# Optimization experiments

Hardware: AMD Instinct MI355X
Metric: run time of the kernel (lower is better)

The kernel has to match this reference:

```python
import jax, jax.numpy as jnp
import numpy as np

EPS = 1e-6        # vn_layers EPS
BN_EPS = 1e-5     # torch BatchNorm eps
NEG = 0.2         # leaky relu negative_slope


def _bcast(v, nd):
    return v.reshape((1, -1) + (1,) * (nd - 2))


def vn_linear_leaky(x, W, D, gamma, beta):
    """VNLinearLeakyReLU: x [B,Cin,3,...], W/D [Cout,Cin] -> [B,Cout,3,...]."""
    p = jnp.einsum('oc,bcv...->bov...', W, x)
    # VNBatchNorm (training-mode batch statistics) on vector norms
    norm = jnp.linalg.norm(p, axis=2) + EPS              # [B,Cout,...]
    axes = (0,) + tuple(range(2, norm.ndim))
    mu = jnp.mean(norm, axis=axes, keepdims=True)
    var = jnp.mean((norm - mu) ** 2, axis=axes, keepdims=True)
    norm_bn = (norm - mu) / jnp.sqrt(var + BN_EPS)
    norm_bn = norm_bn * _bcast(gamma, norm.ndim) + _bcast(beta, norm.ndim)
    p = p / norm[:, :, None] * norm_bn[:, :, None]
    # VN LeakyReLU against learned direction d
    d = jnp.einsum('oc,bcv...->bov...', D, x)
    dot = jnp.sum(p * d, axis=2, keepdims=True)
    mask = (dot >= 0).astype(p.dtype)
    dns = jnp.sum(d * d, axis=2, keepdims=True)
    return NEG * p + (1 - NEG) * (mask * p + (1 - mask) * (p - (dot / (dns + EPS)) * d))


def chnorm(x):
    """channel_equi_vec_normalize: x [B,C,3,...]."""
    n = jnp.linalg.norm(x, axis=2, keepdims=True)        # [B,C,1,...]
    x_dir = x / jnp.maximum(n, 1e-12)
    n_ch = jnp.linalg.norm(n, axis=1, keepdims=True)     # normalize norms over channels
    return x_dir * (n / jnp.maximum(n_ch, 1e-12))


def get_graph_feature(y, k):
    """VN-DGCNN graph feature: y [B,C,3,N] -> [B,2C,3,N,K]."""
    B, C, _, N = y.shape
    yp = jnp.transpose(y, (0, 3, 1, 2))                  # [B,N,C,3]
    flat = yp.reshape(B, N, 3 * C)
    sq = jnp.sum(flat * flat, axis=-1)                   # [B,N]
    inner = jnp.einsum('bnd,bmd->bnm', flat, flat)
    neg_dist = 2 * inner - sq[:, :, None] - sq[:, None, :]
    _, idx = jax.lax.top_k(neg_dist, k)                  # [B,N,K] nearest (incl. self)
    nbr = jax.vmap(lambda pts, ids: pts[ids])(yp, idx)   # [B,N,K,C,3]
    ctr = jnp.broadcast_to(yp[:, :, None], (B, N, k, C, 3))
    feat = jnp.concatenate([nbr - ctr, ctr], axis=3)     # [B,N,K,2C,3]
    return jnp.transpose(feat, (0, 3, 4, 1, 2))


def reference(x, y, Wq, Dq, gq, bq, Wk, Dk, gk, bk, Wv, Dv, gv, bv, k):
    Qx = chnorm(vn_linear_leaky(x, Wq, Dq, gq, bq))      # [B,C,3,N]
    yg = get_graph_feature(y, k)                         # [B,2C,3,N,K]
    Ky = chnorm(vn_linear_leaky(yg, Wk, Dk, gk, bk))     # [B,C,3,N,K]
    Vy = vn_linear_leaky(yg, Wv, Dv, gv, bv)             # [B,C,3,N,K]
    qk = jnp.sum(Ky * Qx[..., None], axis=2)             # [B,C,N,K]
    C = qk.shape[1]
    atten = jax.nn.softmax(qk / jnp.sqrt(jnp.float32(3 * C)), axis=-1)
    return x + jnp.sum(atten[:, :, None] * Vy, axis=-1)  # [B,C,3,N]


def setup_inputs() -> dict:
    key = jax.random.key(0)
    B, C, N, K = 4, 64, 2048, 16
    ks = jax.random.split(key, 8)
    s1 = 1.0 / np.sqrt(C)
    s2 = 1.0 / np.sqrt(2 * C)
    return {
        'x': jax.random.normal(ks[0], (B, C, 3, N), jnp.float32),
        'y': jax.random.normal(ks[1], (B, C, 3, N), jnp.float32),
        'Wq': jax.random.normal(ks[2], (C, C), jnp.float32) * s1,
        'Dq': jax.random.normal(ks[3], (C, C), jnp.float32) * s1,
        'gq': jnp.ones((C,), jnp.float32),
        'bq': jnp.zeros((C,), jnp.float32),
        'Wk': jax.random.normal(ks[4], (C, 2 * C), jnp.float32) * s2,
        'Dk': jax.random.normal(ks[5], (C, 2 * C), jnp.float32) * s2,
        'gk': jnp.ones((C,), jnp.float32),
        'bk': jnp.zeros((C,), jnp.float32),
        'Wv': jax.random.normal(ks[6], (C, 2 * C), jnp.float32) * s2,
        'Dv': jax.random.normal(ks[7], (C, 2 * C), jnp.float32) * s2,
        'gv': jnp.ones((C,), jnp.float32),
        'bv': jnp.zeros((C,), jnp.float32),
        'k': K,
    }
```

## Files before the change

### kernel.cpp

```cpp
#include <hip/hip_runtime.h>
#include <cstdint>
#include <cstddef>

constexpr int B_ = 4, C_ = 64, N_ = 2048, K_ = 16;
constexpr int D3 = 192;
constexpr float EPS_ = 1e-6f, BNE_ = 1e-5f, NEG_ = 0.2f;
constexpr size_t S_ = (size_t)B_ * N_ * D3;

constexpr size_t OFF_PQ  = 0;
constexpr size_t OFF_DQ  = 1*S_;
constexpr size_t OFF_UK  = 2*S_;
constexpr size_t OFF_WK  = 3*S_;
constexpr size_t OFF_UDK = 4*S_;
constexpr size_t OFF_WDK = 5*S_;
constexpr size_t OFF_UV  = 6*S_;
constexpr size_t OFF_WV  = 7*S_;
constexpr size_t OFF_UDV = 8*S_;
constexpr size_t OFF_WDV = 9*S_;
constexpr size_t OFF_SQ  = 10*S_;
constexpr size_t OFF_ST  = OFF_SQ + (size_t)B_*N_;
constexpr size_t OFF_IDX = OFF_ST + 1024;
constexpr size_t OFF_DIST= OFF_IDX + (size_t)B_*N_*K_;

__device__ __forceinline__ float wred_sum(float v) {
  #pragma unroll
  for (int off = 32; off > 0; off >>= 1) v += __shfl_xor(v, off, 64);
  return v;
}

__device__ __forceinline__ void vnlk(float& p0, float& p1, float& p2,
                                     float d0, float d1, float d2,
                                     float s, float sh) {
  float n2 = p0*p0 + p1*p1 + p2*p2;
  float norm = __builtin_amdgcn_sqrtf(n2) + EPS_;
  float f = fmaf(norm, s, sh) * __builtin_amdgcn_rcpf(norm);
  p0 *= f; p1 *= f; p2 *= f;
  float dot = p0*d0 + p1*d1 + p2*d2;
  float dns = d0*d0 + d1*d1 + d2*d2;
  float g = (1.f - NEG_) * fminf(dot, 0.f) * __builtin_amdgcn_rcpf(dns + EPS_);
  p0 = fmaf(-g, d0, p0); p1 = fmaf(-g, d1, p1); p2 = fmaf(-g, d2, p2);
}

__device__ __forceinline__ float chnorm_sc(float nc, float nch) {
  return nc * __builtin_amdgcn_rcpf(fmaxf(nc, 1e-12f))
            * __builtin_amdgcn_rcpf(fmaxf(nch, 1e-12f));
}

template<bool PAIR>
__device__ __forceinline__ void do_mm(const float (*ys)[36], const float (*Wl)[129],
                                      float* __restrict__ out0, float* __restrict__ out1,
                                      float* s1s, float* s2s, bool qs,
                                      int og, int ng, int b, int n0) {
  float accU[4][2][3] = {};
  float accW[4][2][3] = {};
  #pragma unroll 4
  for (int c = 0; c < 64; ++c) {
    float w1[4], wd[4];
    #pragma unroll
    for (int i = 0; i < 4; ++i) {
      w1[i] = Wl[og*4 + i][c];
      if (PAIR) wd[i] = Wl[og*4 + i][64 + c] - w1[i];
    }
    #pragma unroll
    for (int jj = 0; jj < 2; ++jj)
      #pragma unroll
      for (int v = 0; v < 3; ++v) {
        float yv = ys[c*3 + v][ng*2 + jj];
        #pragma unroll
        for (int i = 0; i < 4; ++i) {
          accU[i][jj][v] = fmaf(w1[i], yv, accU[i][jj][v]);
          if (PAIR) accW[i][jj][v] = fmaf(wd[i], yv, accW[i][jj][v]);
        }
      }
  }
  #pragma unroll
  for (int jj = 0; jj < 2; ++jj) {
    int n = n0 + ng*2 + jj;
    size_t base = ((size_t)b*N_ + n)*D3 + og*12;
    alignas(16) float tmp[12];
    #pragma unroll
    for (int i = 0; i < 4; ++i)
      #pragma unroll
      for (int v = 0; v < 3; ++v) tmp[i*3+v] = accU[i][jj][v];
    float4* dst = (float4*)(out0 + base);
    dst[0] = ((float4*)tmp)[0]; dst[1] = ((float4*)tmp)[1]; dst[2] = ((float4*)tmp)[2];
    if (PAIR) {
      #pragma unroll
      for (int i = 0; i < 4; ++i)
        #pragma unroll
        for (int v = 0; v < 3; ++v) tmp[i*3+v] = accW[i][jj][v];
      float4* dst1 = (float4*)(out1 + base);
      dst1[0] = ((float4*)tmp)[0]; dst1[1] = ((float4*)tmp)[1]; dst1[2] = ((float4*)tmp)[2];
    }
  }
  if (!PAIR && qs) {
    #pragma unroll
    for (int i = 0; i < 4; ++i) {
      float a = 0.f, b2 = 0.f;
      #pragma unroll
      for (int jj = 0; jj < 2; ++jj) {
        float nn = sqrtf(accU[i][jj][0]*accU[i][jj][0] + accU[i][jj][1]*accU[i][jj][1]
                       + accU[i][jj][2]*accU[i][jj][2]) + EPS_;
        a += nn; b2 += nn*nn;
      }
      atomicAdd(&s1s[og*4 + i], a);
      atomicAdd(&s2s[og*4 + i], b2);
    }
  }
}

__global__ __launch_bounds__(256) void transform_kernel(
    const float* __restrict__ x, const float* __restrict__ y,
    const float* __restrict__ Wq, const float* __restrict__ Dq,
    const float* __restrict__ Wk, const float* __restrict__ Dk,
    const float* __restrict__ Wv, const float* __restrict__ Dv,
    float* __restrict__ ws) {
  __shared__ float ys[D3][36];
  __shared__ float Wl[64][129];
  __shared__ float s1s[64], s2s[64];
  int t = threadIdx.x, n0 = blockIdx.x*32, b = blockIdx.y, z = blockIdx.z;
  const bool isx = (z < 2);
  const float* in = (isx ? x : y) + (size_t)b*D3*N_;
  #pragma unroll
  for (int i = 0; i < 6; ++i) {
    int lin = t + i*256;
    int d = lin >> 3, c4 = (lin & 7)*4;
    *(float4*)&ys[d][c4] = *(const float4*)&in[(size_t)d*N_ + n0 + c4];
  }
  const float* Wg = (z==0)?Wq:(z==1)?Dq:(z==2)?Wk:(z==3)?Dk:(z==4)?Wv:Dv;
  if (isx) { for (int i = t; i < 4096; i += 256) Wl[i>>6][i&63] = Wg[i]; }
  else     { for (int i = t; i < 8192; i += 256) Wl[i>>7][i&127] = Wg[i]; }
  if (z == 0 && t < 64) { s1s[t] = 0.f; s2s[t] = 0.f; }
  __syncthreads();
  if (z == 2 && t < 32) {
    float s = 0.f;
    for (int d = 0; d < D3; ++d) { float v = ys[d][t]; s += v*v; }
    ws[OFF_SQ + (size_t)b*N_ + n0 + t] = s;
  }
  int og = t & 15, ng = t >> 4;
  float* st = ws + OFF_ST;
  if (isx) {
    float* out0 = ws + (z ? OFF_DQ : OFF_PQ);
    do_mm<false>(ys, Wl, out0, nullptr, s1s, s2s, z == 0, og, ng, b, n0);
    if (z == 0) {
      __syncthreads();
      if (t < 64) { atomicAdd(&st[t], s1s[t]); atomicAdd(&st[64 + t], s2s[t]); }
    }
  } else {
    float* out0 = ws + ((z==2)?OFF_UK:(z==3)?OFF_UDK:(z==4)?OFF_UV:OFF_UDV);
    float* out1 = ws + ((z==2)?OFF_WK:(z==3)?OFF_WDK:(z==4)?OFF_WV:OFF_WDV);
    do_mm<true>(ys, Wl, out0, out1, nullptr, nullptr, false, og, ng, b, n0);
  }
}

__global__ __launch_bounds__(256) void dist_kernel(const float* __restrict__ y,
                                                   float* __restrict__ ws,
                                                   int b0, size_t dstride) {
  __shared__ float As[32][68];
  __shared__ float Bs[32][136];
  int b = b0 + blockIdx.z;
  const float* yb = y + (size_t)b * D3 * N_;
  const float* sq = ws + OFF_SQ + (size_t)b * N_;
  float* dist = ws + OFF_DIST + dstride * blockIdx.z;
  int t = threadIdx.x;
  int m0 = blockIdx.x * 128, n0 = blockIdx.y * 64;
  int tm = t & 15, tn = t >> 4;
  float acc[4][8] = {};
  for (int dt = 0; dt < 6; ++dt) {
    __syncthreads();
    #pragma unroll
    for (int i = 0; i < 2; ++i) {
      int idx = t + i*256;
      int dd = idx >> 4, c4 = (idx & 15)*4;
      *(float4*)&As[dd][c4] = *(const float4*)&yb[(size_t)(dt*32 + dd)*N_ + n0 + c4];
    }
    #pragma unroll
    for (int i = 0; i < 4; ++i) {
      int idx = t + i*256;
      int dd = idx >> 5, c4 = (idx & 31)*4;
      *(float4*)&Bs[dd][c4] = *(const float4*)&yb[(size_t)(dt*32 + dd)*N_ + m0 + c4];
    }
    __syncthreads();
    #pragma unroll 8
    for (int dd = 0; dd < 32; ++dd) {
      float4 a4 = *(float4*)&As[dd][tn*4];
      float4 b4 = *(float4*)&Bs[dd][tm*4];
      float4 c4 = *(float4*)&Bs[dd][64 + tm*4];
      float ar[4] = {a4.x, a4.y, a4.z, a4.w};
      float b0v[4] = {b4.x, b4.y, b4.z, b4.w};
      float b1v[4] = {c4.x, c4.y, c4.z, c4.w};
      #pragma unroll
      for (int j = 0; j < 4; ++j) {
        #pragma unroll
        for (int i = 0; i < 4; ++i) {
          acc[j][i]   = fmaf(ar[j], b0v[i], acc[j][i]);
          acc[j][4+i] = fmaf(ar[j], b1v[i], acc[j][4+i]);
        }
      }
    }
  }
  float4 s0 = *(const float4*)&sq[m0 + tm*4];
  float4 s1 = *(const float4*)&sq[m0 + 64 + tm*4];
  float sm0[4] = {s0.x, s0.y, s0.z, s0.w};
  float sm1[4] = {s1.x, s1.y, s1.z, s1.w};
  #pragma unroll
  for (int j = 0; j < 4; ++j) {
    float sn = sq[n0 + tn*4 + j];
    float4 r0, r1;
    r0.x = 2.f*acc[j][0] - sn - sm0[0]; r0.y = 2.f*acc[j][1] - sn - sm0[1];
    r0.z = 2.f*acc[j][2] - sn - sm0[2]; r0.w = 2.f*acc[j][3] - sn - sm0[3];
    r1.x = 2.f*acc[j][4] - sn - sm1[0]; r1.y = 2.f*acc[j][5] - sn - sm1[1];
    r1.z = 2.f*acc[j][6] - sn - sm1[2]; r1.w = 2.f*acc[j][7] - sn - sm1[3];
    size_t rowb = (size_t)(n0 + tn*4 + j)*N_ + m0 + tm*4;
    *(float4*)&dist[rowb]      = r0;
    *(float4*)&dist[rowb + 64] = r1;
  }
}

__global__ __launch_bounds__(256) void topk_kernel(const float* __restrict__ ws_c,
                                                   int* __restrict__ idxo,
                                                   int b0, size_t dstride) {
  int t = threadIdx.x;
  int w = t >> 6, l = t & 63;
  int n = blockIdx.x*4 + w;
  int b = b0 + blockIdx.y;
  const float* dr = ws_c + OFF_DIST + dstride*blockIdx.y + (size_t)n * N_;
  float v[32];
  #pragma unroll
  for (int j = 0; j < 32; ++j) v[j] = dr[j*64 + l];
  int mine = 0;
  for (int it = 0; it < K_; ++it) {
    float bv = v[0]; int bj = 0;
    #pragma unroll
    for (int j = 1; j < 32; ++j) {
      bool g = v[j] > bv;
      bv = g ? v[j] : bv;
      bj = g ? j : bj;
    }
    int bm = bj*64 + l;
    #pragma unroll
    for (int off = 32; off > 0; off >>= 1) {
      float ov = __shfl_xor(bv, off, 64);
      int   om = __shfl_xor(bm, off, 64);
      if (ov > bv || (ov == bv && om < bm)) { bv = ov; bm = om; }
    }
    if (l == it) mine = bm;
    int wj = bm >> 6, wl = bm & 63;
    #pragma unroll
    for (int j = 0; j < 32; ++j)
      v[j] = (j == wj && l == wl) ? -3.4e38f : v[j];
  }
  if (l < K_) idxo[((size_t)b*N_ + n)*K_ + l] = mine;
}

__global__ __launch_bounds__(256) void kvstats_kernel(float* __restrict__ ws,
                                                      const int* __restrict__ idxp) {
  int t = threadIdx.x, o = t & 63, eg = t >> 6;
  int e0 = blockIdx.x * 128, b = blockIdx.y;
  const float* uK = ws + OFF_UK; const float* wK = ws + OFF_WK;
  const float* uV = ws + OFF_UV; const float* wV = ws + OFF_WV;
  int bN = b * N_;
  float k1 = 0.f, k2 = 0.f, v1 = 0.f, v2 = 0.f;
  for (int j = 0; j < 32; ++j) {
    int e = e0 + eg + j*4;
    int n = e >> 4, kk = e & 15;
    int m = idxp[(bN + n)*K_ + kk];
    int rb = (bN + n)*D3 + o*3;
    int gb = (bN + m)*D3 + o*3;
    float p0 = uK[gb] + wK[rb], p1 = uK[gb+1] + wK[rb+1], p2 = uK[gb+2] + wK[rb+2];
    float nk = __builtin_amdgcn_sqrtf(p0*p0 + p1*p1 + p2*p2) + EPS_;
    k1 += nk; k2 += nk*nk;
    float q0 = uV[gb] + wV[rb], q1 = uV[gb+1] + wV[rb+1], q2 = uV[gb+2] + wV[rb+2];
    float nv = __builtin_amdgcn_sqrtf(q0*q0 + q1*q1 + q2*q2) + EPS_;
    v1 += nv; v2 += nv*nv;
  }
  __shared__ float red[4][256];
  red[0][t] = k1; red[1][t] = k2; red[2][t] = v1; red[3][t] = v2;
  __syncthreads();
  if (t < 64) {
    float* st = ws + OFF_ST;
    float a = red[0][t] + red[0][t+64] + red[0][t+128] + red[0][t+192];
    atomicAdd(&st[128 + t], a);
    a = red[1][t] + red[1][t+64] + red[1][t+128] + red[1][t+192];
    atomicAdd(&st[192 + t], a);
    a = red[2][t] + red[2][t+64] + red[2][t+128] + red[2][t+192];
    atomicAdd(&st[256 + t], a);
    a = red[3][t] + red[3][t+64] + red[3][t+128] + red[3][t+192];
    atomicAdd(&st[320 + t], a);
  }
}

__global__ void bn_finalize(const float* __restrict__ gq, const float* __restrict__ bq,
                            const float* __restrict__ gk, const float* __restrict__ bk,
                            const float* __restrict__ gv, const float* __restrict__ bv,
                            float* __restrict__ ws) {
  int o = threadIdx.x;
  if (o >= 64) return;
  float* st = ws + OFF_ST;
  float cq = (float)(B_ * N_);
  float mu = st[o] / cq;
  float var = fmaxf(st[64+o]/cq - mu*mu, 0.f);
  float s = gq[o] * rsqrtf(var + BNE_);
  st[384+o] = s; st[448+o] = bq[o] - mu*s;
  float ck = (float)(B_ * N_ * K_);
  mu = st[128+o] / ck;
  var = fmaxf(st[192+o]/ck - mu*mu, 0.f);
  s = gk[o] * rsqrtf(var + BNE_);
  st[512+o] = s; st[576+o] = bk[o] - mu*s;
  mu = st[256+o] / ck;
  var = fmaxf(st[320+o]/ck - mu*mu, 0.f);
  s = gv[o] * rsqrtf(var + BNE_);
  st[640+o] = s; st[704+o] = bv[o] - mu*s;
}

__global__ __launch_bounds__(256, 2) void final_kernel(const float* __restrict__ x,
                                                       const float* __restrict__ ws_c,
                                                       const int* __restrict__ idxp,
                                                       float* __restrict__ out) {
  const float* pq  = ws_c + OFF_PQ;  const float* dq  = ws_c + OFF_DQ;
  const float* uK  = ws_c + OFF_UK;  const float* wK  = ws_c + OFF_WK;
  const float* uDk = ws_c + OFF_UDK; const float* wDk = ws_c + OFF_WDK;
  const float* uV  = ws_c + OFF_UV;  const float* wV  = ws_c + OFF_WV;
  const float* uDv = ws_c + OFF_UDV; const float* wDv = ws_c + OFF_WDV;
  const float* st  = ws_c + OFF_ST;
  int t = threadIdx.x, o = t & 63, w = t >> 6;
  int n0 = blockIdx.x*4, n = n0 + w, b = blockIdx.y;
  int bN = b * N_;
  __shared__ float ob2[192][5];
  int mi[16];
  {
    const int* ip = idxp + (size_t)(bN + n)*K_;
    int4 a0 = *(const int4*)&ip[0];  mi[0]=a0.x;  mi[1]=a0.y;  mi[2]=a0.z;  mi[3]=a0.w;
    int4 a1 = *(const int4*)&ip[4];  mi[4]=a1.x;  mi[5]=a1.y;  mi[6]=a1.z;  mi[7]=a1.w;
    int4 a2 = *(const int4*)&ip[8];  mi[8]=a2.x;  mi[9]=a2.y;  mi[10]=a2.z; mi[11]=a2.w;
    int4 a3 = *(const int4*)&ip[12]; mi[12]=a3.x; mi[13]=a3.y; mi[14]=a3.z; mi[15]=a3.w;
  }
  int rb = (bN + n)*D3 + o*3;
  float q0 = pq[rb], q1 = pq[rb+1], q2 = pq[rb+2];
  float e0 = dq[rb], e1 = dq[rb+1], e2 = dq[rb+2];
  vnlk(q0, q1, q2, e0, e1, e2, st[384+o], st[448+o]);
  float qn2 = q0*q0 + q1*q1 + q2*q2;
  float qsc = chnorm_sc(__builtin_amdgcn_sqrtf(qn2),
                        __builtin_amdgcn_sqrtf(wred_sum(qn2)));
  float qx0 = q0*qsc, qx1 = q1*qsc, qx2 = q2*qsc;
  float wk0 = wK[rb],  wk1 = wK[rb+1],  wk2 = wK[rb+2];
  float wdk0= wDk[rb], wdk1= wDk[rb+1], wdk2= wDk[rb+2];
  float sK = st[512+o], shK = st[576+o], sV = st[640+o], shV = st[704+o];
  const float isq = 0.07216878364870323f;
  float qk[16];
  #pragma unroll
  for (int kk = 0; kk < 16; ++kk) {
    int gb = (bN + mi[kk])*D3 + o*3;
    float p0 = uK[gb] + wk0, p1 = uK[gb+1] + wk1, p2 = uK[gb+2] + wk2;
    float f0 = uDk[gb] + wdk0, f1 = uDk[gb+1] + wdk1, f2 = uDk[gb+2] + wdk2;
    vnlk(p0, p1, p2, f0, f1, f2, sK, shK);
    float nc2 = p0*p0 + p1*p1 + p2*p2;
    float sc = chnorm_sc(__builtin_amdgcn_sqrtf(nc2),
                         __builtin_amdgcn_sqrtf(wred_sum(nc2)));
    qk[kk] = (p0*qx0 + p1*qx1 + p2*qx2) * (sc * isq);
  }
  float mx = qk[0];
  #pragma unroll
  for (int kk = 1; kk < 16; ++kk) mx = fmaxf(mx, qk[kk]);
  float se = 0.f;
  #pragma unroll
  for (int kk = 0; kk < 16; ++kk) { float e = __expf(qk[kk] - mx); qk[kk] = e; se += e; }
  float inv = __builtin_amdgcn_rcpf(se);
  float wv0 = wV[rb],  wv1 = wV[rb+1],  wv2 = wV[rb+2];
  float wdv0= wDv[rb], wdv1= wDv[rb+1], wdv2= wDv[rb+2];
  float a0 = 0.f, a1 = 0.f, a2 = 0.f;
  #pragma unroll
  for (int kk = 0; kk < 16; ++kk) {
    int gb = (bN + mi[kk])*D3 + o*3;
    float v0 = uV[gb] + wv0, v1 = uV[gb+1] + wv1, v2 = uV[gb+2] + wv2;
    float g0 = uDv[gb] + wdv0, g1 = uDv[gb+1] + wdv1, g2 = uDv[gb+2] + wdv2;
    vnlk(v0, v1, v2, g0, g1, g2, sV, shV);
    float at = qk[kk] * inv;
    a0 = fmaf(at, v0, a0); a1 = fmaf(at, v1, a1); a2 = fmaf(at, v2, a2);
  }
  ob2[o*3 + 0][w] = a0;
  ob2[o*3 + 1][w] = a1;
  ob2[o*3 + 2][w] = a2;
  __syncthreads();
  if (t < 192) {
    size_t xo = ((size_t)b*D3 + t)*N_ + n0;
    float4 xr = *(const float4*)&x[xo];
    float4 r;
    r.x = xr.x + ob2[t][0]; r.y = xr.y + ob2[t][1];
    r.z = xr.z + ob2[t][2]; r.w = xr.w + ob2[t][3];
    *(float4*)&out[xo] = r;
  }
}

extern "C" void kernel_launch(void* const* d_in, const int* in_sizes, int n_in,
                              void* d_out, int out_size, void* d_ws, size_t ws_size,
                              hipStream_t stream) {
  const float* x  = (const float*)d_in[0];
  const float* y  = (const float*)d_in[1];
  const float* Wq = (const float*)d_in[2];
  const float* Dq = (const float*)d_in[3];
  const float* gq = (const float*)d_in[4];
  const float* bq = (const float*)d_in[5];
  const float* Wk = (const float*)d_in[6];
  const float* Dk = (const float*)d_in[7];
  const float* gk = (const float*)d_in[8];
  const float* bk = (const float*)d_in[9];
  const float* Wv = (const float*)d_in[10];
  const float* Dv = (const float*)d_in[11];
  const float* gv = (const float*)d_in[12];
  const float* bv = (const float*)d_in[13];
  float* ws = (float*)d_ws;
  float* out = (float*)d_out;
  int* idxp = (int*)(ws + OFF_IDX);

  const size_t need = (OFF_DIST + (size_t)B_*N_*N_) * sizeof(float);
  const bool batched = ws_size >= need;

  hipMemsetAsync((void*)(ws + OFF_ST), 0, 1024 * sizeof(float), stream);
  transform_kernel<<<dim3(N_/32, B_, 6), 256, 0, stream>>>(x, y, Wq, Dq, Wk, Dk, Wv, Dv, ws);
  if (batched) {
    dist_kernel<<<dim3(N_/128, N_/64, B_), 256, 0, stream>>>(y, ws, 0, (size_t)N_*N_);
    topk_kernel<<<dim3(N_/4, B_), 256, 0, stream>>>(ws, idxp, 0, (size_t)N_*N_);
  } else {
    for (int b = 0; b < B_; ++b) {
      dist_kernel<<<dim3(N_/128, N_/64, 1), 256, 0, stream>>>(y, ws, b, 0);
      topk_kernel<<<dim3(N_/4, 1), 256, 0, stream>>>(ws, idxp, b, 0);
    }
  }
  kvstats_kernel<<<dim3(N_*K_/128, B_), 256, 0, stream>>>(ws, idxp);
  bn_finalize<<<1, 64, 0, stream>>>(gq, bq, gk, bk, gv, bv, ws);
  final_kernel<<<dim3(N_/4, B_), 256, 0, stream>>>(x, ws, idxp, out);
}
```

Baseline: 358.0 us.

## Interleave gathered K/V features, prefetch dist tiles, fold BN finalize into final

The four per-neighbor gathered feature arrays (uK, uDk, uV, uDv) are stored interleaved in one row of 768 floats per point, so each neighbor gather in final_kernel and kvstats touches one contiguous region instead of four separate arrays. The distance GEMM now prefetches the next tile of global loads into registers while computing the current tile. The bn_finalize launch is removed and each final_kernel thread computes the batch-norm scale and shift itself. The trade-offs are some redundant per-thread BN arithmetic and higher register pressure in dist_kernel.

After: 377.5 us. 1.05x slower.

```diff
diff --git a/kernel.cpp b/kernel.cpp
--- a/kernel.cpp
+++ b/kernel.cpp
@@ -9,13 +9,10 @@
 
 constexpr size_t OFF_PQ  = 0;
 constexpr size_t OFF_DQ  = 1*S_;
-constexpr size_t OFF_UK  = 2*S_;
-constexpr size_t OFF_WK  = 3*S_;
-constexpr size_t OFF_UDK = 4*S_;
-constexpr size_t OFF_WDK = 5*S_;
-constexpr size_t OFF_UV  = 6*S_;
-constexpr size_t OFF_WV  = 7*S_;
-constexpr size_t OFF_UDV = 8*S_;
+constexpr size_t OFF_GB  = 2*S_;
+constexpr size_t OFF_WK  = 6*S_;
+constexpr size_t OFF_WDK = 7*S_;
+constexpr size_t OFF_WV  = 8*S_;
 constexpr size_t OFF_WDV = 9*S_;
 constexpr size_t OFF_SQ  = 10*S_;
 constexpr size_t OFF_ST  = OFF_SQ + (size_t)B_*N_;
@@ -50,7 +47,7 @@
 __device__ __forceinline__ void do_mm(const float (*ys)[36], const float (*Wl)[129],
                                       float* __restrict__ out0, float* __restrict__ out1,
                                       float* s1s, float* s2s, bool qs,
-                                      int og, int ng, int b, int n0) {
+                                      int og, int ng, int b, int n0, int rs0) {
   float accU[4][2][3] = {};
   float accW[4][2][3] = {};
   #pragma unroll 4
@@ -76,20 +73,21 @@
   #pragma unroll
   for (int jj = 0; jj < 2; ++jj) {
     int n = n0 + ng*2 + jj;
-    size_t base = ((size_t)b*N_ + n)*D3 + og*12;
+    size_t base0 = ((size_t)b*N_ + n)*rs0 + og*12;
     alignas(16) float tmp[12];
     #pragma unroll
     for (int i = 0; i < 4; ++i)
       #pragma unroll
       for (int v = 0; v < 3; ++v) tmp[i*3+v] = accU[i][jj][v];
-    float4* dst = (float4*)(out0 + base);
+    float4* dst = (float4*)(out0 + base0);
     dst[0] = ((float4*)tmp)[0]; dst[1] = ((float4*)tmp)[1]; dst[2] = ((float4*)tmp)[2];
     if (PAIR) {
+      size_t base1 = ((size_t)b*N_ + n)*D3 + og*12;
       #pragma unroll
       for (int i = 0; i < 4; ++i)
         #pragma unroll
         for (int v = 0; v < 3; ++v) tmp[i*3+v] = accW[i][jj][v];
-      float4* dst1 = (float4*)(out1 + base);
+      float4* dst1 = (float4*)(out1 + base1);
       dst1[0] = ((float4*)tmp)[0]; dst1[1] = ((float4*)tmp)[1]; dst1[2] = ((float4*)tmp)[2];
     }
   }
@@ -141,15 +139,16 @@
   float* st = ws + OFF_ST;
   if (isx) {
     float* out0 = ws + (z ? OFF_DQ : OFF_PQ);
-    do_mm<false>(ys, Wl, out0, nullptr, s1s, s2s, z == 0, og, ng, b, n0);
+    do_mm<false>(ys, Wl, out0, nullptr, s1s, s2s, z == 0, og, ng, b, n0, D3);
     if (z == 0) {
       __syncthreads();
       if (t < 64) { atomicAdd(&st[t], s1s[t]); atomicAdd(&st[64 + t], s2s[t]); }
     }
   } else {
-    float* out0 = ws + ((z==2)?OFF_UK:(z==3)?OFF_UDK:(z==4)?OFF_UV:OFF_UDV);
+    int seg = z - 2;
+    float* out0 = ws + OFF_GB + (size_t)seg*192;
     float* out1 = ws + ((z==2)?OFF_WK:(z==3)?OFF_WDK:(z==4)?OFF_WV:OFF_WDV);
-    do_mm<true>(ys, Wl, out0, out1, nullptr, nullptr, false, og, ng, b, n0);
+    do_mm<true>(ys, Wl, out0, out1, nullptr, nullptr, false, og, ng, b, n0, 768);
   }
 }
 
@@ -166,21 +165,42 @@
   int m0 = blockIdx.x * 128, n0 = blockIdx.y * 64;
   int tm = t & 15, tn = t >> 4;
   float acc[4][8] = {};
+  float4 pa[2], pb[4];
+  #pragma unroll
+  for (int i = 0; i < 2; ++i) {
+    int idx = t + i*256;
+    pa[i] = *(const float4*)&yb[(size_t)(idx >> 4)*N_ + n0 + (idx & 15)*4];
+  }
+  #pragma unroll
+  for (int i = 0; i < 4; ++i) {
+    int idx = t + i*256;
+    pb[i] = *(const float4*)&yb[(size_t)(idx >> 5)*N_ + m0 + (idx & 31)*4];
+  }
   for (int dt = 0; dt < 6; ++dt) {
     __syncthreads();
     #pragma unroll
     for (int i = 0; i < 2; ++i) {
       int idx = t + i*256;
-      int dd = idx >> 4, c4 = (idx & 15)*4;
-      *(float4*)&As[dd][c4] = *(const float4*)&yb[(size_t)(dt*32 + dd)*N_ + n0 + c4];
+      *(float4*)&As[idx >> 4][(idx & 15)*4] = pa[i];
     }
     #pragma unroll
     for (int i = 0; i < 4; ++i) {
       int idx = t + i*256;
-      int dd = idx >> 5, c4 = (idx & 31)*4;
-      *(float4*)&Bs[dd][c4] = *(const float4*)&yb[(size_t)(dt*32 + dd)*N_ + m0 + c4];
+      *(float4*)&Bs[idx >> 5][(idx & 31)*4] = pb[i];
     }
     __syncthreads();
+    if (dt < 5) {
+      #pragma unroll
+      for (int i = 0; i < 2; ++i) {
+        int idx = t + i*256;
+        pa[i] = *(const float4*)&yb[(size_t)((dt+1)*32 + (idx >> 4))*N_ + n0 + (idx & 15)*4];
+      }
+      #pragma unroll
+      for (int i = 0; i < 4; ++i) {
+        int idx = t + i*256;
+        pb[i] = *(const float4*)&yb[(size_t)((dt+1)*32 + (idx >> 5))*N_ + m0 + (idx & 31)*4];
+      }
+    }
     #pragma unroll 8
     for (int dd = 0; dd < 32; ++dd) {
       float4 a4 = *(float4*)&As[dd][tn*4];
@@ -257,8 +277,8 @@
                                                       const int* __restrict__ idxp) {
   int t = threadIdx.x, o = t & 63, eg = t >> 6;
   int e0 = blockIdx.x * 128, b = blockIdx.y;
-  const float* uK = ws + OFF_UK; const float* wK = ws + OFF_WK;
-  const float* uV = ws + OFF_UV; const float* wV = ws + OFF_WV;
+  const float* GB = ws + OFF_GB;
+  const float* wK = ws + OFF_WK; const float* wV = ws + OFF_WV;
   int bN = b * N_;
   float k1 = 0.f, k2 = 0.f, v1 = 0.f, v2 = 0.f;
   for (int j = 0; j < 32; ++j) {
@@ -266,11 +286,11 @@
     int n = e >> 4, kk = e & 15;
     int m = idxp[(bN + n)*K_ + kk];
     int rb = (bN + n)*D3 + o*3;
-    int gb = (bN + m)*D3 + o*3;
-    float p0 = uK[gb] + wK[rb], p1 = uK[gb+1] + wK[rb+1], p2 = uK[gb+2] + wK[rb+2];
+    size_t gb = (size_t)(bN + m)*768 + o*3;
+    float p0 = GB[gb] + wK[rb], p1 = GB[gb+1] + wK[rb+1], p2 = GB[gb+2] + wK[rb+2];
     float nk = __builtin_amdgcn_sqrtf(p0*p0 + p1*p1 + p2*p2) + EPS_;
     k1 += nk; k2 += nk*nk;
-    float q0 = uV[gb] + wV[rb], q1 = uV[gb+1] + wV[rb+1], q2 = uV[gb+2] + wV[rb+2];
+    float q0 = GB[gb+384] + wV[rb], q1 = GB[gb+385] + wV[rb+1], q2 = GB[gb+386] + wV[rb+2];
     float nv = __builtin_amdgcn_sqrtf(q0*q0 + q1*q1 + q2*q2) + EPS_;
     v1 += nv; v2 += nv*nv;
   }
@@ -290,43 +310,39 @@
   }
 }
 
-__global__ void bn_finalize(const float* __restrict__ gq, const float* __restrict__ bq,
-                            const float* __restrict__ gk, const float* __restrict__ bk,
-                            const float* __restrict__ gv, const float* __restrict__ bv,
-                            float* __restrict__ ws) {
-  int o = threadIdx.x;
-  if (o >= 64) return;
-  float* st = ws + OFF_ST;
-  float cq = (float)(B_ * N_);
-  float mu = st[o] / cq;
-  float var = fmaxf(st[64+o]/cq - mu*mu, 0.f);
-  float s = gq[o] * rsqrtf(var + BNE_);
-  st[384+o] = s; st[448+o] = bq[o] - mu*s;
-  float ck = (float)(B_ * N_ * K_);
-  mu = st[128+o] / ck;
-  var = fmaxf(st[192+o]/ck - mu*mu, 0.f);
-  s = gk[o] * rsqrtf(var + BNE_);
-  st[512+o] = s; st[576+o] = bk[o] - mu*s;
-  mu = st[256+o] / ck;
-  var = fmaxf(st[320+o]/ck - mu*mu, 0.f);
-  s = gv[o] * rsqrtf(var + BNE_);
-  st[640+o] = s; st[704+o] = bv[o] - mu*s;
-}
-
 __global__ __launch_bounds__(256, 2) void final_kernel(const float* __restrict__ x,
                                                        const float* __restrict__ ws_c,
                                                        const int* __restrict__ idxp,
+                                                       const float* __restrict__ gq,
+                                                       const float* __restrict__ bq,
+                                                       const float* __restrict__ gk,
+                                                       const float* __restrict__ bk,
+                                                       const float* __restrict__ gv,
+                                                       const float* __restrict__ bv,
                                                        float* __restrict__ out) {
   const float* pq  = ws_c + OFF_PQ;  const float* dq  = ws_c + OFF_DQ;
-  const float* uK  = ws_c + OFF_UK;  const float* wK  = ws_c + OFF_WK;
-  const float* uDk = ws_c + OFF_UDK; const float* wDk = ws_c + OFF_WDK;
-  const float* uV  = ws_c + OFF_UV;  const float* wV  = ws_c + OFF_WV;
-  const float* uDv = ws_c + OFF_UDV; const float* wDv = ws_c + OFF_WDV;
+  const float* GB  = ws_c + OFF_GB;
+  const float* wK  = ws_c + OFF_WK;  const float* wDk = ws_c + OFF_WDK;
+  const float* wV  = ws_c + OFF_WV;  const float* wDv = ws_c + OFF_WDV;
   const float* st  = ws_c + OFF_ST;
   int t = threadIdx.x, o = t & 63, w = t >> 6;
   int n0 = blockIdx.x*4, n = n0 + w, b = blockIdx.y;
   int bN = b * N_;
   __shared__ float ob2[192][5];
+  float sQ, shQ, sK, shK, sV, shV;
+  {
+    const float icq = 1.f / (float)(B_ * N_);
+    float mu = st[o] * icq;
+    float var = fmaxf(st[64+o]*icq - mu*mu, 0.f);
+    sQ = gq[o] * rsqrtf(var + BNE_); shQ = bq[o] - mu*sQ;
+    const float ick = 1.f / (float)(B_ * N_ * K_);
+    mu = st[128+o] * ick;
+    var = fmaxf(st[192+o]*ick - mu*mu, 0.f);
+    sK = gk[o] * rsqrtf(var + BNE_); shK = bk[o] - mu*sK;
+    mu = st[256+o] * ick;
+    var = fmaxf(st[320+o]*ick - mu*mu, 0.f);
+    sV = gv[o] * rsqrtf(var + BNE_); shV = bv[o] - mu*sV;
+  }
   int mi[16];
   {
     const int* ip = idxp + (size_t)(bN + n)*K_;
@@ -338,21 +354,20 @@
   int rb = (bN + n)*D3 + o*3;
   float q0 = pq[rb], q1 = pq[rb+1], q2 = pq[rb+2];
   float e0 = dq[rb], e1 = dq[rb+1], e2 = dq[rb+2];
-  vnlk(q0, q1, q2, e0, e1, e2, st[384+o], st[448+o]);
+  vnlk(q0, q1, q2, e0, e1, e2, sQ, shQ);
   float qn2 = q0*q0 + q1*q1 + q2*q2;
   float qsc = chnorm_sc(__builtin_amdgcn_sqrtf(qn2),
                         __builtin_amdgcn_sqrtf(wred_sum(qn2)));
   float qx0 = q0*qsc, qx1 = q1*qsc, qx2 = q2*qsc;
   float wk0 = wK[rb],  wk1 = wK[rb+1],  wk2 = wK[rb+2];
   float wdk0= wDk[rb], wdk1= wDk[rb+1], wdk2= wDk[rb+2];
-  float sK = st[512+o], shK = st[576+o], sV = st[640+o], shV = st[704+o];
   const float isq = 0.07216878364870323f;
   float qk[16];
   #pragma unroll
   for (int kk = 0; kk < 16; ++kk) {
-    int gb = (bN + mi[kk])*D3 + o*3;
-    float p0 = uK[gb] + wk0, p1 = uK[gb+1] + wk1, p2 = uK[gb+2] + wk2;
-    float f0 = uDk[gb] + wdk0, f1 = uDk[gb+1] + wdk1, f2 = uDk[gb+2] + wdk2;
+    size_t gb = (size_t)(bN + mi[kk])*768 + o*3;
+    float p0 = GB[gb]     + wk0, p1 = GB[gb+1]   + wk1, p2 = GB[gb+2]   + wk2;
+    float f0 = GB[gb+192] + wdk0, f1 = GB[gb+193] + wdk1, f2 = GB[gb+194] + wdk2;
     vnlk(p0, p1, p2, f0, f1, f2, sK, shK);
     float nc2 = p0*p0 + p1*p1 + p2*p2;
     float sc = chnorm_sc(__builtin_amdgcn_sqrtf(nc2),
@@ -371,9 +386,9 @@
   float a0 = 0.f, a1 = 0.f, a2 = 0.f;
   #pragma unroll
   for (int kk = 0; kk < 16; ++kk) {
-    int gb = (bN + mi[kk])*D3 + o*3;
-    float v0 = uV[gb] + wv0, v1 = uV[gb+1] + wv1, v2 = uV[gb+2] + wv2;
-    float g0 = uDv[gb] + wdv0, g1 = uDv[gb+1] + wdv1, g2 = uDv[gb+2] + wdv2;
+    size_t gb = (size_t)(bN + mi[kk])*768 + o*3;
+    float v0 = GB[gb+384] + wv0, v1 = GB[gb+385] + wv1, v2 = GB[gb+386] + wv2;
+    float g0 = GB[gb+576] + wdv0, g1 = GB[gb+577] + wdv1, g2 = GB[gb+578] + wdv2;
     vnlk(v0, v1, v2, g0, g1, g2, sV, shV);
     float at = qk[kk] * inv;
     a0 = fmaf(at, v0, a0); a1 = fmaf(at, v1, a1); a2 = fmaf(at, v2, a2);
@@ -428,6 +443,5 @@
     }
   }
   kvstats_kernel<<<dim3(N_*K_/128, B_), 256, 0, stream>>>(ws, idxp);
-  bn_finalize<<<1, 64, 0, stream>>>(gq, bq, gk, bk, gv, bv, ws);
-  final_kernel<<<dim3(N_/4, B_), 256, 0, stream>>>(x, ws, idxp, out);
-}
+  final_kernel<<<dim3(N_/4, B_), 256, 0, stream>>>(x, ws, idxp, gq, bq, gk, bk, gv, bv, out);
+}
```
